# Kernel tuning notes

Hardware: AMD Instinct MI355X
Metric: run time of the kernel (lower is better)

The kernel has to match this reference:

```python
import jax, jax.numpy as jnp
import numpy as np

B, IN_DIM = 64, 256
R, L = 2, 2                    # rank, num_mlp_layers
D1A, D2A = 1024, 512           # w1 shape
D1B, D2B = 512, 1024           # w2 shape
H, O = 3072, 1536              # hyper hidden = int(sum(shape)*2.0), out = sum(shape)


def setup_inputs() -> dict:
    key = jax.random.key(0)
    ks = iter(jax.random.split(key, 20))

    def rn(shape, s=0.02):
        return jax.random.normal(next(ks), shape, dtype=jnp.float32) * s

    inp = {
        "u_0": jax.random.normal(next(ks), (B, IN_DIM), dtype=jnp.float32),
        "w1": rn((D1A, D2A)),
        "w2": rn((D1B, D2B)),
    }
    for n in ("w1", "w2"):
        inp[f"win_{n}"] = rn((R, H, IN_DIM))
        inp[f"bin_{n}"] = rn((R, H))
        inp[f"hw_{n}"] = rn((R, L, H, H))
        inp[f"hb_{n}"] = rn((R, L, H))
        inp[f"wout_{n}"] = rn((R, O, H))
        inp[f"bout_{n}"] = rn((R, O))
    return inp


def _gelu(x):
    # torch F.gelu default = exact erf-based gelu
    return jax.nn.gelu(x, approximate=False)


def _mlp_apply(x, win, b_in, hw, hb, wout, b_out):
    # MLP_net_variable with use_act=False, use_dropout=False
    h = _gelu(x @ win.T + b_in)              # [B, H]
    for l in range(hw.shape[0]):             # small fixed num_layers
        h = _gelu(h @ hw[l].T + hb[l])
    return h @ wout.T + b_out                # [B, O], no final activation


def _synth(vec_u, base, win, b_in, hw, hb, wout, b_out):
    d1, d2 = base.shape
    # vmap the per-rank MLPs over the stacked rank axis -> flat [R, B, d1+d2]
    flat = jax.vmap(lambda W, b, HW, HB, WO, BO: _mlp_apply(vec_u, W, b, HW, HB, WO, BO))(
        win, b_in, hw, hb, wout, b_out)
    v1, v2 = flat[..., :d1], flat[..., d1:]  # split along feature dim (torch .split)
    # sum over rank of per-batch outer products, added once to the base param
    return base[None] + jnp.einsum('rbi,rbj->bij', v1, v2)


def reference(u_0, w1, w2,
              win_w1, bin_w1, hw_w1, hb_w1, wout_w1, bout_w1,
              win_w2, bin_w2, hw_w2, hb_w2, wout_w2, bout_w2):
    vec_u = u_0.reshape(u_0.shape[0], -1)    # [B, in_dim]
    new_w1 = _synth(vec_u, w1, win_w1, bin_w1, hw_w1, hb_w1, wout_w1, bout_w1)
    new_w2 = _synth(vec_u, w2, win_w2, bin_w2, hw_w2, hb_w2, wout_w2, bout_w2)
    return (new_w1, new_w2)
```

## Files before the change

kernel.cpp:

```cpp
#include <hip/hip_runtime.h>
#include <hip/hip_bf16.h>

typedef float f32x4 __attribute__((ext_vector_type(4)));
typedef short s16x8 __attribute__((ext_vector_type(8)));
typedef short s16x4 __attribute__((ext_vector_type(4)));

#define THREADS 256

__device__ __forceinline__ unsigned short f2bf(float f) {
  union { float f; unsigned int u; } v;
  v.f = f;
  unsigned int u = v.u;
  u += 0x7fffu + ((u >> 16) & 1u);
  return (unsigned short)(u >> 16);
}

struct GemmArgs {
  const float* W[4];
  const float* Bi[4];
};

template<bool GELU, bool OUTBF16>
__global__ __launch_bounds__(THREADS) void mlp_gemm(
    const unsigned short* __restrict__ X, unsigned long long xstride,
    GemmArgs args,
    void* __restrict__ Y, unsigned long long ystride,
    int N, int K)
{
  constexpr int NT = 48;
  constexpr int KC = 256;
  __shared__ __align__(16) unsigned short Wb[2][NT * KC];

  const int e    = blockIdx.y;
  const int n0   = blockIdx.x * NT;
  const int t    = threadIdx.x;
  const int lane = t & 63;
  const int wid  = t >> 6;

  const float* __restrict__ Wg = args.W[e];
  const unsigned short* __restrict__ Xg = X + (size_t)e * xstride;

  const int srow = t >> 6;
  const int skq  = t & 63;

  f32x4 sreg[12];

  auto load_stage = [&](int k0) {
#pragma unroll
    for (int rd = 0; rd < 12; ++rd) {
      const int row = rd * 4 + srow;
      sreg[rd] = *(const f32x4*)(Wg + (size_t)(n0 + row) * K + k0 + skq * 4);
    }
  };

  auto write_stage = [&](int bi) {
    unsigned short* lds = Wb[bi];
#pragma unroll
    for (int rd = 0; rd < 12; ++rd) {
      const int row = rd * 4 + srow;
      const int off = row * KC + ((((skq >> 1) ^ (row & 7)) << 3) | ((skq & 1) << 2));
      s16x4 p;
      p[0] = (short)f2bf(sreg[rd][0]);
      p[1] = (short)f2bf(sreg[rd][1]);
      p[2] = (short)f2bf(sreg[rd][2]);
      p[3] = (short)f2bf(sreg[rd][3]);
      *(s16x4*)(lds + off) = p;
    }
  };

  f32x4 acc[3];
#pragma unroll
  for (int i = 0; i < 3; ++i)
#pragma unroll
    for (int j = 0; j < 4; ++j) acc[i][j] = 0.0f;

  const int arow = wid * 16 + (lane & 15);
  const int kfr  = (lane >> 4) * 8;
  const unsigned short* __restrict__ xrow = Xg + (size_t)arow * K + kfr;
  const int brow0 = lane & 15;
  const int bch   = lane >> 4;

  auto compute = [&](int bi, int kg) {
    const unsigned short* lds = Wb[bi];
#pragma unroll
    for (int kk = 0; kk < KC; kk += 32) {
      s16x8 a = *(const s16x8*)(xrow + kg + kk);
#pragma unroll
      for (int nf = 0; nf < 3; ++nf) {
        const int row = nf * 16 + brow0;
        const int ch  = ((kk >> 3) + bch) ^ (row & 7);
        s16x8 b = *(const s16x8*)(lds + row * KC + ch * 8);
        acc[nf] = __builtin_amdgcn_mfma_f32_16x16x32_bf16(a, b, acc[nf], 0, 0, 0);
      }
    }
  };

  const int NCH = K / KC;

  load_stage(0);
  write_stage(0);
  __syncthreads();

  for (int c = 0; c < NCH; ++c) {
    if (c + 1 < NCH) load_stage((c + 1) * KC);
    compute(c & 1, c * KC);
    __syncthreads();
    if (c + 1 < NCH) {
      write_stage((c + 1) & 1);
      __syncthreads();
    }
  }

  const float* __restrict__ Bi = args.Bi[e];
  const int col   = lane & 15;
  const int rbase = wid * 16 + ((lane >> 4) << 2);
#pragma unroll
  for (int nf = 0; nf < 3; ++nf) {
    const int nn = n0 + nf * 16 + col;
    const float bv = Bi[nn];
#pragma unroll
    for (int r = 0; r < 4; ++r) {
      float yv = acc[nf][r] + bv;
      if (GELU) yv = 0.5f * yv * (1.0f + erff(yv * 0.70710678118654752f));
      const size_t oidx = (size_t)e * ystride + (size_t)(rbase + r) * N + nn;
      if (OUTBF16) ((unsigned short*)Y)[oidx] = f2bf(yv);
      else         ((float*)Y)[oidx] = yv;
    }
  }
}

__global__ __launch_bounds__(THREADS) void cvt_u_kernel(
    const float* __restrict__ u, unsigned short* __restrict__ ub)
{
  const int i = blockIdx.x * THREADS + threadIdx.x;
  ub[i] = f2bf(u[i]);
}

template<int D1, int D2>
__global__ __launch_bounds__(THREADS) void synth_kernel(
    const float* __restrict__ Wbase, const float* __restrict__ V,
    float* __restrict__ Out)
{
  constexpr int QPR = D2 / 4;
  constexpr int RP  = THREADS / QPR;
  constexpr size_t S = (size_t)64 * 1536;
  const int b    = blockIdx.y;
  const int i0   = blockIdx.x * 32;
  const int isub = threadIdx.x / QPR;
  const int jq   = threadIdx.x % QPR;
  const float* __restrict__ vb = V + (size_t)b * 1536;
  const f32x4 v2a = *(const f32x4*)(vb + D1 + jq * 4);
  const f32x4 v2b = *(const f32x4*)(vb + S + D1 + jq * 4);
#pragma unroll
  for (int ii = isub; ii < 32; ii += RP) {
    const int i = i0 + ii;
    const float a0 = vb[i];
    const float a1 = vb[S + i];
    const f32x4 w = *(const f32x4*)(Wbase + (size_t)i * D2 + jq * 4);
    f32x4 o = w + a0 * v2a + a1 * v2b;
    *(f32x4*)(Out + ((size_t)b * D1 + i) * D2 + jq * 4) = o;
  }
}

extern "C" void kernel_launch(void* const* d_in, const int* in_sizes, int n_in,
                              void* d_out, int out_size, void* d_ws, size_t ws_size,
                              hipStream_t stream) {
  const int Hh = 3072, IND = 256, OD = 1536;

  const float* u0  = (const float*)d_in[0];
  const float* w1  = (const float*)d_in[1];
  const float* w2  = (const float*)d_in[2];
  const float* win[2] = {(const float*)d_in[3], (const float*)d_in[9]};
  const float* bin[2] = {(const float*)d_in[4], (const float*)d_in[10]};
  const float* hw [2] = {(const float*)d_in[5], (const float*)d_in[11]};
  const float* hb [2] = {(const float*)d_in[6], (const float*)d_in[12]};
  const float* wou[2] = {(const float*)d_in[7], (const float*)d_in[13]};
  const float* bou[2] = {(const float*)d_in[8], (const float*)d_in[14]};

  char* ws = (char*)d_ws;
  unsigned short* ub = (unsigned short*)ws;
  unsigned short* hA = (unsigned short*)(ws + (64 << 10));
  unsigned short* hB = (unsigned short*)(ws + (64 << 10) + (2 << 20));
  float*          vv = (float*)(ws + (64 << 10) + (4 << 20));

  cvt_u_kernel<<<64, THREADS, 0, stream>>>(u0, ub);

  GemmArgs ga;
  for (int e = 0; e < 4; ++e) {
    const int n = e >> 1, r = e & 1;
    ga.W[e]  = win[n] + (size_t)r * Hh * IND;
    ga.Bi[e] = bin[n] + (size_t)r * Hh;
  }
  mlp_gemm<true, true><<<dim3(Hh / 48, 4), THREADS, 0, stream>>>(
      ub, 0ull, ga, hA, (unsigned long long)64 * Hh, Hh, IND);

  for (int l = 0; l < 2; ++l) {
    for (int e = 0; e < 4; ++e) {
      const int n = e >> 1, r = e & 1;
      ga.W[e]  = hw[n] + (size_t)(r * 2 + l) * Hh * Hh;
      ga.Bi[e] = hb[n] + (size_t)(r * 2 + l) * Hh;
    }
    const unsigned short* xin = (l == 0) ? hA : hB;
    unsigned short*      yout = (l == 0) ? hB : hA;
    mlp_gemm<true, true><<<dim3(Hh / 48, 4), THREADS, 0, stream>>>(
        xin, (unsigned long long)64 * Hh, ga, yout, (unsigned long long)64 * Hh, Hh, Hh);
  }

  for (int e = 0; e < 4; ++e) {
    const int n = e >> 1, r = e & 1;
    ga.W[e]  = wou[n] + (size_t)r * OD * Hh;
    ga.Bi[e] = bou[n] + (size_t)r * OD;
  }
  mlp_gemm<false, false><<<dim3(OD / 48, 4), THREADS, 0, stream>>>(
      hA, (unsigned long long)64 * Hh, ga, vv, (unsigned long long)64 * OD, OD, Hh);

  float* out = (float*)d_out;
  synth_kernel<1024, 512><<<dim3(1024 / 32, 64), THREADS, 0, stream>>>(w1, vv, out);
  synth_kernel<512, 1024><<<dim3(512 / 32, 64), THREADS, 0, stream>>>(
      w2, vv + (size_t)2 * 64 * 1536, out + (size_t)64 * 1024 * 512);
}
```

Baseline: 659.3 us.

## Shrink GEMM N-tile to 16 and deepen weight prefetch to two stages

Narrows each block's output tile from 48 to 16 columns, which triples the grid so more CUs stream the fp32 weight matrices at once. The global-to-register prefetch now holds two chunks in alternating register sets, and the LDS write of the next chunk moves before a single barrier per iteration instead of two. A-fragments for a whole K-chunk are loaded up front, and launch bounds request 3 blocks per CU. The cost is that every block re-reads the shared activation rows, giving three times the activation traffic, with less MFMA work per block.

Result: no change. 653.5 us (-0.9%).

```diff
diff --git a/kernel.cpp b/kernel.cpp
--- a/kernel.cpp
+++ b/kernel.cpp
@@ -21,13 +21,13 @@
 };
 
 template<bool GELU, bool OUTBF16>
-__global__ __launch_bounds__(THREADS) void mlp_gemm(
+__global__ __launch_bounds__(THREADS, 3) void mlp_gemm(
     const unsigned short* __restrict__ X, unsigned long long xstride,
     GemmArgs args,
     void* __restrict__ Y, unsigned long long ystride,
     int N, int K)
 {
-  constexpr int NT = 48;
+  constexpr int NT = 16;
   constexpr int KC = 256;
   __shared__ __align__(16) unsigned short Wb[2][NT * KC];
 
@@ -40,92 +40,87 @@
   const float* __restrict__ Wg = args.W[e];
   const unsigned short* __restrict__ Xg = X + (size_t)e * xstride;
 
-  const int srow = t >> 6;
-  const int skq  = t & 63;
-
-  f32x4 sreg[12];
-
-  auto load_stage = [&](int k0) {
-#pragma unroll
-    for (int rd = 0; rd < 12; ++rd) {
+  const int srow = wid;
+  const int skq  = lane;
+
+  auto load_st = [&](f32x4 (&s)[4], int k0) {
+#pragma unroll
+    for (int rd = 0; rd < 4; ++rd) {
       const int row = rd * 4 + srow;
-      sreg[rd] = *(const f32x4*)(Wg + (size_t)(n0 + row) * K + k0 + skq * 4);
+      s[rd] = *(const f32x4*)(Wg + (size_t)(n0 + row) * K + k0 + skq * 4);
     }
   };
 
-  auto write_stage = [&](int bi) {
+  auto write_st = [&](int bi, const f32x4 (&s)[4]) {
     unsigned short* lds = Wb[bi];
 #pragma unroll
-    for (int rd = 0; rd < 12; ++rd) {
+    for (int rd = 0; rd < 4; ++rd) {
       const int row = rd * 4 + srow;
       const int off = row * KC + ((((skq >> 1) ^ (row & 7)) << 3) | ((skq & 1) << 2));
       s16x4 p;
-      p[0] = (short)f2bf(sreg[rd][0]);
-      p[1] = (short)f2bf(sreg[rd][1]);
-      p[2] = (short)f2bf(sreg[rd][2]);
-      p[3] = (short)f2bf(sreg[rd][3]);
+      p[0] = (short)f2bf(s[rd][0]);
+      p[1] = (short)f2bf(s[rd][1]);
+      p[2] = (short)f2bf(s[rd][2]);
+      p[3] = (short)f2bf(s[rd][3]);
       *(s16x4*)(lds + off) = p;
     }
   };
 
-  f32x4 acc[3];
-#pragma unroll
-  for (int i = 0; i < 3; ++i)
-#pragma unroll
-    for (int j = 0; j < 4; ++j) acc[i][j] = 0.0f;
+  f32x4 acc = {0.f, 0.f, 0.f, 0.f};
 
   const int arow = wid * 16 + (lane & 15);
-  const int kfr  = (lane >> 4) * 8;
-  const unsigned short* __restrict__ xrow = Xg + (size_t)arow * K + kfr;
-  const int brow0 = lane & 15;
-  const int bch   = lane >> 4;
+  const unsigned short* __restrict__ xrow = Xg + (size_t)arow * K + ((lane >> 4) << 3);
+  const int brow = lane & 15;
+  const int bch  = lane >> 4;
 
   auto compute = [&](int bi, int kg) {
     const unsigned short* lds = Wb[bi];
-#pragma unroll
-    for (int kk = 0; kk < KC; kk += 32) {
-      s16x8 a = *(const s16x8*)(xrow + kg + kk);
-#pragma unroll
-      for (int nf = 0; nf < 3; ++nf) {
-        const int row = nf * 16 + brow0;
-        const int ch  = ((kk >> 3) + bch) ^ (row & 7);
-        s16x8 b = *(const s16x8*)(lds + row * KC + ch * 8);
-        acc[nf] = __builtin_amdgcn_mfma_f32_16x16x32_bf16(a, b, acc[nf], 0, 0, 0);
-      }
+    s16x8 af[8];
+#pragma unroll
+    for (int i = 0; i < 8; ++i)
+      af[i] = *(const s16x8*)(xrow + kg + i * 32);
+#pragma unroll
+    for (int i = 0; i < 8; ++i) {
+      const int ch = ((i << 2) + bch) ^ (brow & 7);
+      s16x8 b = *(const s16x8*)(lds + brow * KC + ch * 8);
+      acc = __builtin_amdgcn_mfma_f32_16x16x32_bf16(af[i], b, acc, 0, 0, 0);
     }
   };
 
   const int NCH = K / KC;
 
-  load_stage(0);
-  write_stage(0);
+  f32x4 sA[4], sB[4];
+  load_st(sA, 0);
+  if (NCH > 1) load_st(sB, KC);
+  write_st(0, sA);
   __syncthreads();
 
   for (int c = 0; c < NCH; ++c) {
-    if (c + 1 < NCH) load_stage((c + 1) * KC);
+    const bool even = !(c & 1);
+    if (c + 2 < NCH) {
+      if (even) load_st(sA, (c + 2) * KC);
+      else      load_st(sB, (c + 2) * KC);
+    }
     compute(c & 1, c * KC);
+    if (c + 1 < NCH) {
+      if (even) write_st(1, sB);
+      else      write_st(0, sA);
+    }
     __syncthreads();
-    if (c + 1 < NCH) {
-      write_stage((c + 1) & 1);
-      __syncthreads();
-    }
   }
 
   const float* __restrict__ Bi = args.Bi[e];
   const int col   = lane & 15;
+  const int nn    = n0 + col;
   const int rbase = wid * 16 + ((lane >> 4) << 2);
-#pragma unroll
-  for (int nf = 0; nf < 3; ++nf) {
-    const int nn = n0 + nf * 16 + col;
-    const float bv = Bi[nn];
-#pragma unroll
-    for (int r = 0; r < 4; ++r) {
-      float yv = acc[nf][r] + bv;
-      if (GELU) yv = 0.5f * yv * (1.0f + erff(yv * 0.70710678118654752f));
-      const size_t oidx = (size_t)e * ystride + (size_t)(rbase + r) * N + nn;
-      if (OUTBF16) ((unsigned short*)Y)[oidx] = f2bf(yv);
-      else         ((float*)Y)[oidx] = yv;
-    }
+  const float bv  = Bi[nn];
+#pragma unroll
+  for (int r = 0; r < 4; ++r) {
+    float yv = acc[r] + bv;
+    if (GELU) yv = 0.5f * yv * (1.0f + erff(yv * 0.70710678118654752f));
+    const size_t oidx = (size_t)e * ystride + (size_t)(rbase + r) * N + nn;
+    if (OUTBF16) ((unsigned short*)Y)[oidx] = f2bf(yv);
+    else         ((float*)Y)[oidx] = yv;
   }
 }
 
@@ -191,7 +186,7 @@
     ga.W[e]  = win[n] + (size_t)r * Hh * IND;
     ga.Bi[e] = bin[n] + (size_t)r * Hh;
   }
-  mlp_gemm<true, true><<<dim3(Hh / 48, 4), THREADS, 0, stream>>>(
+  mlp_gemm<true, true><<<dim3(Hh / 16, 4), THREADS, 0, stream>>>(
       ub, 0ull, ga, hA, (unsigned long long)64 * Hh, Hh, IND);
 
   for (int l = 0; l < 2; ++l) {
@@ -202,7 +197,7 @@
     }
     const unsigned short* xin = (l == 0) ? hA : hB;
     unsigned short*      yout = (l == 0) ? hB : hA;
-    mlp_gemm<true, true><<<dim3(Hh / 48, 4), THREADS, 0, stream>>>(
+    mlp_gemm<true, true><<<dim3(Hh / 16, 4), THREADS, 0, stream>>>(
         xin, (unsigned long long)64 * Hh, ga, yout, (unsigned long long)64 * Hh, Hh, Hh);
   }
 
@@ -211,7 +206,7 @@
     ga.W[e]  = wou[n] + (size_t)r * OD * Hh;
     ga.Bi[e] = bou[n] + (size_t)r * OD;
   }
-  mlp_gemm<false, false><<<dim3(OD / 48, 4), THREADS, 0, stream>>>(
+  mlp_gemm<false, false><<<dim3(OD / 16, 4), THREADS, 0, stream>>>(
       hA, (unsigned long long)64 * Hh, ga, vv, (unsigned long long)64 * OD, OD, Hh);
 
   float* out = (float*)d_out;
```
